# Kernel tuning notes

Hardware: AMD Instinct MI355X
Metric: run time of the kernel (lower is better)

## Reference

```python
import jax, jax.numpy as jnp
import numpy as np

N_EMBD = 1024
N_HEAD = 16
HEAD_DIM = N_EMBD // N_HEAD
B, T = 8, 1024


def setup_inputs() -> dict:
    key = jax.random.key(0)
    k1, k2, k3, k4 = jax.random.split(key, 4)
    x = jax.random.normal(k1, (B, T, N_EMBD), dtype=jnp.float32)
    # nn.Linear weight shapes: qkv (3C, C) no bias; proj (C, C) with bias
    w_qkv = jax.random.normal(k2, (3 * N_EMBD, N_EMBD), dtype=jnp.float32) * 0.02
    w_proj = jax.random.normal(k3, (N_EMBD, N_EMBD), dtype=jnp.float32) * 0.02
    b_proj = jax.random.normal(k4, (N_EMBD,), dtype=jnp.float32) * 0.02
    return {"x": x, "w_qkv": w_qkv, "w_proj": w_proj, "b_proj": b_proj}


def reference(x, w_qkv, w_proj, b_proj):
    Bq, Tq, C = x.shape
    qkv = jnp.einsum('btc,dc->btd', x, w_qkv)  # (B,T,3C)
    q, k, v = jnp.split(qkv, 3, axis=-1)
    def heads(t):
        return t.reshape(Bq, Tq, N_HEAD, HEAD_DIM).transpose(0, 2, 1, 3)  # (B,H,T,D)
    q, k, v = heads(q), heads(k), heads(v)
    scale = 1.0 / np.sqrt(HEAD_DIM).astype(np.float32)
    att = jnp.einsum('bhqd,bhkd->bhqk', q, k) * scale  # (B,H,T,T)
    causal = jnp.tril(jnp.ones((Tq, Tq), dtype=bool))
    att = jnp.where(causal, att, -jnp.inf)
    att = jax.nn.softmax(att, axis=-1)
    # dropout: eval mode -> identity
    y = jnp.einsum('bhqk,bhkd->bhqd', att, v)
    y = y.transpose(0, 2, 1, 3).reshape(Bq, Tq, C)
    return jnp.einsum('btc,dc->btd', y, w_proj) + b_proj
```

## Files before the change

### kernel.cpp

```cpp
#include <hip/hip_runtime.h>
#include <stdint.h>


#define Bn 8
#define Tn 1024
#define Cn 1024
#define Hn 16
#define Dn 64
#define Mn (Bn * Tn)
#define NQKV (3 * Cn)
#define QKS 2048

typedef unsigned short u16;
typedef float f32x4 __attribute__((ext_vector_type(4)));
typedef __bf16 bf16x8 __attribute__((ext_vector_type(8)));
typedef unsigned short ushx8 __attribute__((ext_vector_type(8)));
typedef unsigned short ushx4 __attribute__((ext_vector_type(4)));

__device__ __forceinline__ u16 f2bf(float f) {
  unsigned int u = __float_as_uint(f);
  u += 0x7fffu + ((u >> 16) & 1u);
  return (u16)(u >> 16);
}
__device__ __forceinline__ u16 f2bf_rna(float f) {
  return (u16)((__float_as_uint(f) + 0x8000u) >> 16);
}

__device__ __forceinline__ f32x4 mfma_bf16(ushx8 a, ushx8 b, f32x4 c) {
  return __builtin_amdgcn_mfma_f32_16x16x32_bf16(
      __builtin_bit_cast(bf16x8, a), __builtin_bit_cast(bf16x8, b), c, 0, 0, 0);
}

__device__ __forceinline__ void async16(const u16* g, u16* l) {
  __builtin_amdgcn_global_load_lds(
      (__attribute__((address_space(1))) void*)(void*)g,
      (__attribute__((address_space(3))) void*)l, 16, 0, 0);
}

template <int CTRL>
__device__ __forceinline__ float dppmov(float v) {
  return __builtin_bit_cast(float, __builtin_amdgcn_update_dpp(
      0, __builtin_bit_cast(int, v), CTRL, 0xf, 0xf, true));
}
__device__ __forceinline__ float red16max(float v) {
  v = fmaxf(v, dppmov<0xB1>(v));
  v = fmaxf(v, dppmov<0x4E>(v));
  v = fmaxf(v, dppmov<0x141>(v));
  v = fmaxf(v, dppmov<0x140>(v));
  return v;
}
__device__ __forceinline__ float red16sum(float v) {
  v += dppmov<0xB1>(v);
  v += dppmov<0x4E>(v);
  v += dppmov<0x141>(v);
  v += dppmov<0x140>(v);
  return v;
}

__global__ void cast3_kernel(const float* __restrict__ a, u16* __restrict__ oa, int na4,
                             const float* __restrict__ b, u16* __restrict__ ob, int nb4,
                             const float* __restrict__ c, u16* __restrict__ oc, int nc4) {
  int i = blockIdx.x * blockDim.x + threadIdx.x;
  const float* in;
  u16* out;
  if (i < na4) { in = a; out = oa; }
  else if (i < na4 + nb4) { in = b; out = ob; i -= na4; }
  else if (i < na4 + nb4 + nc4) { in = c; out = oc; i -= na4 + nb4; }
  else return;
  float4 v = ((const float4*)in)[i];
  ushx4 o = { f2bf(v.x), f2bf(v.y), f2bf(v.z), f2bf(v.w) };
  ((ushx4*)out)[i] = o;
}

#define SLOG2E 0.18033688011112042f

template <int MODE>
__device__ __forceinline__ void gemm_body(
    const u16* __restrict__ A, const u16* __restrict__ Bw,
    void* __restrict__ Cout, u16* __restrict__ vt,
    const float* __restrict__ bias) {
  __shared__ alignas(16) u16 lds[36864];

  const int tid = threadIdx.x;
  const int lane = tid & 63;
  const int wv = tid >> 6;
  const int quad = lane >> 4;
  const int l16 = lane & 15;
  const int wr = wv >> 1;
  const int wc = wv & 1;

  const int xcd = blockIdx.x & 7;
  const int loc = blockIdx.x >> 3;
  const int m0 = (xcd * 4 + (loc & 3)) * 256;
  const int n0 = (loc >> 2) * 128;

  const u16* gA = A + (size_t)m0 * Cn;
  const u16* gB = Bw + (size_t)n0 * Cn;

  const int r0s = tid >> 2;
  const int q0s = (tid & 3) ^ ((r0s >> 1) & 3);
  const int c1s = 512 + tid;
  const int r1s = c1s >> 2;
  const int q1s = (c1s & 3) ^ ((r1s >> 1) & 3);
  const int so0 = r0s * Cn + q0s * 8;
  const int so1 = r1s * Cn + q1s * 8;

  auto stageA = [&](int slot, int h) {
    u16* dst = lds + slot * 8192 + tid * 8;
    const u16* src = gA + (h >> 1) * 64 + (h & 1) * 32;
    async16(src + so0, dst);
    async16(src + so1, dst + 4096);
  };
  auto stageB = [&](int slot, int h) {
    u16* dst = lds + 24576 + slot * 4096 + tid * 8;
    const u16* src = gB + (h >> 1) * 64 + (h & 1) * 32;
    async16(src + so0, dst);
  };

  const int sread = (quad ^ ((l16 >> 1) & 3)) * 8;
  const int aoff = (wr * 64 + l16) * 32 + sread;
  const int boff = 24576 + (wc * 64 + l16) * 32 + sread;

  f32x4 acc[4][4];
#pragma unroll
  for (int i = 0; i < 4; ++i)
#pragma unroll
    for (int j = 0; j < 4; ++j) acc[i][j] = (f32x4){0.f, 0.f, 0.f, 0.f};
  ushx8 af[4], bfr[4];

  stageA(0, 0); stageB(0, 0);
  stageA(1, 1); stageB(1, 1);
  asm volatile("s_waitcnt vmcnt(3)" ::: "memory");
  __builtin_amdgcn_s_barrier();
  asm volatile("" ::: "memory");

#define PH(slot, sslot, hd)                                                    \
  {                                                                            \
    const u16* ab_ = lds + (slot) * 8192 + aoff;                               \
    af[0] = *(const ushx8*)(ab_);                                              \
    af[1] = *(const ushx8*)(ab_ + 512);                                        \
    af[2] = *(const ushx8*)(ab_ + 1024);                                       \
    af[3] = *(const ushx8*)(ab_ + 1536);                                       \
    const u16* bb_ = lds + (slot) * 4096 + boff;                               \
    bfr[0] = *(const ushx8*)(bb_);                                             \
    bfr[1] = *(const ushx8*)(bb_ + 512);                                       \
    bfr[2] = *(const ushx8*)(bb_ + 1024);                                      \
    bfr[3] = *(const ushx8*)(bb_ + 1536);                                      \
    stageA((sslot), (hd));                                                     \
    stageB((sslot), (hd));                                                     \
    asm volatile("" ::: "memory");                                             \
    __builtin_amdgcn_s_barrier();                                              \
    asm volatile("s_waitcnt lgkmcnt(0)" ::: "memory");                         \
    __builtin_amdgcn_s_setprio(1);                                             \
    _Pragma("unroll") for (int mi_ = 0; mi_ < 4; ++mi_) {                      \
      _Pragma("unroll") for (int ni_ = 0; ni_ < 4; ++ni_) {                    \
        acc[mi_][ni_] = mfma_bf16(af[mi_], bfr[ni_], acc[mi_][ni_]);           \
      }                                                                        \
    }                                                                          \
    __builtin_amdgcn_s_setprio(0);                                             \
    asm volatile("s_waitcnt vmcnt(3)" ::: "memory");                           \
    asm volatile("" ::: "memory");                                             \
    __builtin_amdgcn_s_barrier();                                              \
    asm volatile("" ::: "memory");                                             \
  }

#pragma unroll 1
  for (int it = 0; it < 5; ++it) {
    const int p = it * 6;
    PH(0, 2, p + 2)
    PH(1, 0, p + 3)
    PH(2, 1, p + 4)
    PH(0, 2, p + 5)
    PH(1, 0, p + 6)
    PH(2, 1, p + 7)
  }
  PH(0, 2, 31)
  PH(1, 0, 31)
#undef PH
  asm volatile("s_waitcnt vmcnt(0)" ::: "memory");

  if constexpr (MODE) {
    if (n0 < 2 * Cn) {
      const float sc = (n0 < Cn) ? SLOG2E : 1.f;
#pragma unroll
      for (int mi = 0; mi < 4; ++mi) {
#pragma unroll
        for (int ni = 0; ni < 4; ++ni) {
          const int col = n0 + wc * 64 + ni * 16 + l16;
          const int row = m0 + wr * 64 + mi * 16 + quad * 4;
#pragma unroll
          for (int i = 0; i < 4; ++i)
            ((u16*)Cout)[(size_t)(row + i) * QKS + col] = f2bf(acc[mi][ni][i] * sc);
        }
      }
    } else {
#pragma unroll
      for (int mi = 0; mi < 4; ++mi) {
#pragma unroll
        for (int ni = 0; ni < 4; ++ni) {
          const int colV = n0 - 2 * Cn + wc * 64 + ni * 16 + l16;
          const int hh = colV >> 6, dd = colV & 63;
          const int row0 = m0 + wr * 64 + mi * 16 + quad * 4;
          const int bb = row0 >> 10, tt = row0 & 1023;
          unsigned int lo = (unsigned int)f2bf(acc[mi][ni][0]) |
                            ((unsigned int)f2bf(acc[mi][ni][1]) << 16);
          unsigned int hi = (unsigned int)f2bf(acc[mi][ni][2]) |
                            ((unsigned int)f2bf(acc[mi][ni][3]) << 16);
          uint2 pk = {lo, hi};
          *(uint2*)&vt[((size_t)(bb * Hn + hh) * Dn + dd) * Tn + tt] = pk;
        }
      }
    }
  } else {
#pragma unroll
    for (int mi = 0; mi < 4; ++mi) {
#pragma unroll
      for (int ni = 0; ni < 4; ++ni) {
        const int col = n0 + wc * 64 + ni * 16 + l16;
        const float bv = bias[col];
        const int row = m0 + wr * 64 + mi * 16 + quad * 4;
#pragma unroll
        for (int i = 0; i < 4; ++i)
          ((float*)Cout)[(size_t)(row + i) * Cn + col] = acc[mi][ni][i] + bv;
      }
    }
  }
}

__global__ __launch_bounds__(512, 4) void gemm_qkv_k(
    const u16* __restrict__ A, const u16* __restrict__ Bw,
    u16* __restrict__ qk, u16* __restrict__ vt) {
  gemm_body<1>(A, Bw, (void*)qk, vt, nullptr);
}
__global__ __launch_bounds__(512, 4) void gemm_proj_k(
    const u16* __restrict__ A, const u16* __restrict__ Bw,
    float* __restrict__ out, const float* __restrict__ bias) {
  gemm_body<0>(A, Bw, (void*)out, nullptr, bias);
}

__global__ __launch_bounds__(512, 4) void attn_kernel(
    const u16* __restrict__ qk, const u16* __restrict__ vt,
    u16* __restrict__ out) {
  const int j = blockIdx.x, h = blockIdx.y, b = blockIdx.z;
  const int tid = threadIdx.x;
  const int lane = tid & 63;
  const int wv = tid >> 6;
  const int quad = lane >> 4;
  const int l16 = lane & 15;

  __shared__ alignas(16) u16 Ks[2][64 * 64];
  __shared__ alignas(16) u16 Vts[2][64 * 64];
  __shared__ alignas(16) u16 Ps[8][16 * 72];

  const u16* qb = qk + (size_t)b * Tn * QKS + h * Dn;
  const u16* kb = qk + (size_t)b * Tn * QKS + Cn + h * Dn;
  const u16* vtb = vt + (size_t)(b * Hn + h) * Dn * Tn;

  const int srow = tid >> 3;
  const int scc = tid & 7;
  const int sgc = scc ^ (srow & 7);
  u16* pswv = Ps[wv];

#pragma unroll 1
  for (int ph = 0; ph < 2; ++ph) {
    const int qt = ph ? (7 - j) : j;
    const int q0w = qt * 128 + wv * 16;
    const int ntiles = 2 * qt + 2;
    const int tdiag = q0w >> 6;

    ushx8 qf[2];
    {
      const u16* qp = qb + (size_t)(q0w + l16) * QKS + quad * 8;
      qf[0] = *(const ushx8*)qp;
      qf[1] = *(const ushx8*)(qp + 32);
    }

    f32x4 o[4];
#pragma unroll
    for (int nt = 0; nt < 4; ++nt) o[nt] = (f32x4){0.f, 0.f, 0.f, 0.f};
    float mrow[4], lrow[4];
#pragma unroll
    for (int i = 0; i < 4; ++i) { mrow[i] = -__builtin_inff(); lrow[i] = 0.f; }

    __syncthreads();

    async16(kb + (size_t)srow * QKS + sgc * 8, Ks[0] + tid * 8);
    async16(vtb + (size_t)srow * Tn + sgc * 8, Vts[0] + tid * 8);

#pragma unroll 1
    for (int t = 0; t < ntiles; ++t) {
      const int kv0 = t * 64;
      const int bi = t & 1;
      __syncthreads();

      if (t + 1 < ntiles) {
        const int nkv0 = kv0 + 64;
        async16(kb + (size_t)(nkv0 + srow) * QKS + sgc * 8, Ks[bi ^ 1] + tid * 8);
        async16(vtb + (size_t)srow * Tn + nkv0 + sgc * 8, Vts[bi ^ 1] + tid * 8);
      }

      if (t > tdiag) continue;

      const u16* ks = Ks[bi];
      const u16* vs = Vts[bi];
      f32x4 s[4];
#pragma unroll
      for (int nt = 0; nt < 4; ++nt) s[nt] = (f32x4){0.f, 0.f, 0.f, 0.f};
#pragma unroll
      for (int nt = 0; nt < 4; ++nt) {
        const int rb = nt * 16 + l16;
        ushx8 b0 = *(const ushx8*)(ks + rb * 64 + (quad ^ (rb & 7)) * 8);
        ushx8 b1 = *(const ushx8*)(ks + rb * 64 + ((quad + 4) ^ (rb & 7)) * 8);
        s[nt] = mfma_bf16(qf[0], b0, s[nt]);
        s[nt] = mfma_bf16(qf[1], b1, s[nt]);
      }

      if (t == tdiag) {
#pragma unroll
        for (int i = 0; i < 4; ++i) {
          const int qr = q0w + quad * 4 + i;
          float vv[4];
          float rmax = -__builtin_inff();
#pragma unroll
          for (int nt = 0; nt < 4; ++nt) {
            float v = s[nt][i];
            if ((kv0 + nt * 16 + l16) > qr) v = -__builtin_inff();
            vv[nt] = v;
            rmax = fmaxf(rmax, v);
          }
          rmax = red16max(rmax);
          const float mnew = fmaxf(mrow[i], rmax);
          const float al = __builtin_amdgcn_exp2f(mrow[i] - mnew);
          mrow[i] = mnew;
          float rsum = 0.f;
#pragma unroll
          for (int nt = 0; nt < 4; ++nt) {
            float p = __builtin_amdgcn_exp2f(vv[nt] - mnew);
            rsum += p;
            pswv[(quad * 4 + i) * 72 + nt * 16 + l16] = f2bf_rna(p);
          }
          lrow[i] = lrow[i] * al + rsum;
#pragma unroll
          for (int nt = 0; nt < 4; ++nt) o[nt][i] *= al;
        }
      } else {
#pragma unroll
        for (int i = 0; i < 4; ++i) {
          float rmax = fmaxf(fmaxf(s[0][i], s[1][i]), fmaxf(s[2][i], s[3][i]));
          rmax = red16max(rmax);
          const float mnew = fmaxf(mrow[i], rmax);
          const float al = __builtin_amdgcn_exp2f(mrow[i] - mnew);
          mrow[i] = mnew;
          float rsum = 0.f;
#pragma unroll
          for (int nt = 0; nt < 4; ++nt) {
            float p = __builtin_amdgcn_exp2f(s[nt][i] - mnew);
            rsum += p;
            pswv[(quad * 4 + i) * 72 + nt * 16 + l16] = f2bf_rna(p);
          }
          lrow[i] = lrow[i] * al + rsum;
#pragma unroll
          for (int nt = 0; nt < 4; ++nt) o[nt][i] *= al;
        }
      }

      ushx8 pf0, pf1;
      {
        const u16* pp = pswv + l16 * 72 + quad * 8;
        pf0 = *(const ushx8*)pp;
        pf1 = *(const ushx8*)(pp + 32);
      }

#pragma unroll
      for (int nt = 0; nt < 4; ++nt) {
        const int rb = nt * 16 + l16;
        ushx8 v0 = *(const ushx8*)(vs + rb * 64 + (quad ^ (rb & 7)) * 8);
        ushx8 v1 = *(const ushx8*)(vs + rb * 64 + ((quad + 4) ^ (rb & 7)) * 8);
        o[nt] = mfma_bf16(pf0, v0, o[nt]);
        o[nt] = mfma_bf16(pf1, v1, o[nt]);
      }
    }

#pragma unroll
    for (int i = 0; i < 4; ++i) {
      const float inv = 1.f / red16sum(lrow[i]);
      const int trow = q0w + quad * 4 + i;
      u16* op = out + ((size_t)(b * Tn + trow)) * Cn + h * Dn + l16;
#pragma unroll
      for (int nt = 0; nt < 4; ++nt) op[nt * 16] = f2bf(o[nt][i] * inv);
    }
  }
}

extern "C" void kernel_launch(void* const* d_in, const int* in_sizes, int n_in,
                              void* d_out, int out_size, void* d_ws, size_t ws_size,
                              hipStream_t stream) {
  const float* x = (const float*)d_in[0];
  const float* w_qkv = (const float*)d_in[1];
  const float* w_proj = (const float*)d_in[2];
  const float* b_proj = (const float*)d_in[3];
  float* out = (float*)d_out;
  char* ws = (char*)d_ws;

  u16* xb     = (u16*)(ws);
  u16* wqkvb  = (u16*)(ws + 16777216);
  u16* wprojb = (u16*)(ws + 23068672);
  u16* qkb    = (u16*)(ws + 25165824);
  u16* vtb    = (u16*)(ws + 58720256);
  u16* yb     = (u16*)(ws + 75497472);

  cast3_kernel<<<12288, 256, 0, stream>>>(x, xb, 2097152,
                                          w_qkv, wqkvb, 786432,
                                          w_proj, wprojb, 262144);

  gemm_qkv_k<<<768, 512, 0, stream>>>(xb, wqkvb, qkb, vtb);

  attn_kernel<<<dim3(4, Hn, Bn), 512, 0, stream>>>(qkb, vtb, yb);

  gemm_proj_k<<<256, 512, 0, stream>>>(yb, wprojb, out, b_proj);
}
```

Before: 224.3 us.

## Use 4-wave GEMM blocks with larger per-wave tiles and smaller proj tiles

```diff
diff --git a/kernel.cpp b/kernel.cpp
--- a/kernel.cpp
+++ b/kernel.cpp
@@ -74,12 +74,22 @@
 
 #define SLOG2E 0.18033688011112042f
 
-template <int MODE>
-__device__ __forceinline__ void gemm_body(
+template <int BM, int MODE>
+__device__ __forceinline__ void gemm_body4(
     const u16* __restrict__ A, const u16* __restrict__ Bw,
     void* __restrict__ Cout, u16* __restrict__ vt,
     const float* __restrict__ bias) {
-  __shared__ alignas(16) u16 lds[36864];
+  constexpr int ASLOT = BM * 32;
+  constexpr int BSLOT = 128 * 32;
+  constexpr int BBASE = 3 * ASLOT;
+  constexpr int ASW = BM / 64;
+  constexpr int BSW = 2;
+  constexpr int LOADS = ASW + BSW;
+  constexpr int MREP = BM / 32;
+  constexpr int MT = Mn / BM;
+  constexpr int MPX = MT / 8;
+
+  __shared__ alignas(16) u16 lds[3 * (ASLOT + BSLOT)];
 
   const int tid = threadIdx.x;
   const int lane = tid & 63;
@@ -91,74 +101,73 @@
 
   const int xcd = blockIdx.x & 7;
   const int loc = blockIdx.x >> 3;
-  const int m0 = (xcd * 4 + (loc & 3)) * 256;
-  const int n0 = (loc >> 2) * 128;
+  const int m0 = (xcd * MPX + (loc & (MPX - 1))) * BM;
+  const int n0 = (loc / MPX) * 128;
 
   const u16* gA = A + (size_t)m0 * Cn;
   const u16* gB = Bw + (size_t)n0 * Cn;
 
-  const int r0s = tid >> 2;
-  const int q0s = (tid & 3) ^ ((r0s >> 1) & 3);
-  const int c1s = 512 + tid;
-  const int r1s = c1s >> 2;
-  const int q1s = (c1s & 3) ^ ((r1s >> 1) & 3);
-  const int so0 = r0s * Cn + q0s * 8;
-  const int so1 = r1s * Cn + q1s * 8;
-
-  auto stageA = [&](int slot, int h) {
-    u16* dst = lds + slot * 8192 + tid * 8;
-    const u16* src = gA + (h >> 1) * 64 + (h & 1) * 32;
-    async16(src + so0, dst);
-    async16(src + so1, dst + 4096);
+  int soff[4];
+#pragma unroll
+  for (int s = 0; s < 4; ++s) {
+    int c = s * 256 + tid;
+    int row = c >> 2;
+    int q = (c & 3) ^ ((row >> 1) & 3);
+    soff[s] = row * Cn + q * 8;
+  }
+
+  auto stage = [&](int slot, int h) {
+    const u16* sA = gA + (h >> 1) * 64 + (h & 1) * 32;
+    u16* dA = lds + slot * ASLOT + tid * 8;
+#pragma unroll
+    for (int s = 0; s < ASW; ++s) async16(sA + soff[s], dA + s * 2048);
+    const u16* sB = gB + (h >> 1) * 64 + (h & 1) * 32;
+    u16* dB = lds + BBASE + slot * BSLOT + tid * 8;
+#pragma unroll
+    for (int s = 0; s < BSW; ++s) async16(sB + soff[s], dB + s * 2048);
   };
-  auto stageB = [&](int slot, int h) {
-    u16* dst = lds + 24576 + slot * 4096 + tid * 8;
-    const u16* src = gB + (h >> 1) * 64 + (h & 1) * 32;
-    async16(src + so0, dst);
-  };
 
   const int sread = (quad ^ ((l16 >> 1) & 3)) * 8;
-  const int aoff = (wr * 64 + l16) * 32 + sread;
-  const int boff = 24576 + (wc * 64 + l16) * 32 + sread;
-
-  f32x4 acc[4][4];
-#pragma unroll
-  for (int i = 0; i < 4; ++i)
+  const int aoff = (wr * (BM / 2) + l16) * 32 + sread;
+  const int boff = BBASE + (wc * 64 + l16) * 32 + sread;
+
+  f32x4 acc[MREP][4];
+#pragma unroll
+  for (int i = 0; i < MREP; ++i)
 #pragma unroll
     for (int j = 0; j < 4; ++j) acc[i][j] = (f32x4){0.f, 0.f, 0.f, 0.f};
-  ushx8 af[4], bfr[4];
-
-  stageA(0, 0); stageB(0, 0);
-  stageA(1, 1); stageB(1, 1);
-  asm volatile("s_waitcnt vmcnt(3)" ::: "memory");
+  ushx8 af[MREP], bfr[4];
+
+  stage(0, 0);
+  stage(1, 1);
+  if constexpr (LOADS == 6) asm volatile("s_waitcnt vmcnt(6)" ::: "memory");
+  else asm volatile("s_waitcnt vmcnt(4)" ::: "memory");
   __builtin_amdgcn_s_barrier();
   asm volatile("" ::: "memory");
 
 #define PH(slot, sslot, hd)                                                    \
   {                                                                            \
-    const u16* ab_ = lds + (slot) * 8192 + aoff;                               \
-    af[0] = *(const ushx8*)(ab_);                                              \
-    af[1] = *(const ushx8*)(ab_ + 512);                                        \
-    af[2] = *(const ushx8*)(ab_ + 1024);                                       \
-    af[3] = *(const ushx8*)(ab_ + 1536);                                       \
-    const u16* bb_ = lds + (slot) * 4096 + boff;                               \
-    bfr[0] = *(const ushx8*)(bb_);                                             \
-    bfr[1] = *(const ushx8*)(bb_ + 512);                                       \
-    bfr[2] = *(const ushx8*)(bb_ + 1024);                                      \
-    bfr[3] = *(const ushx8*)(bb_ + 1536);                                      \
-    stageA((sslot), (hd));                                                     \
-    stageB((sslot), (hd));                                                     \
+    const u16* ab_ = lds + (slot) * ASLOT + aoff;                              \
+    _Pragma("unroll") for (int mi_ = 0; mi_ < MREP; ++mi_)                     \
+      af[mi_] = *(const ushx8*)(ab_ + mi_ * 512);                              \
+    const u16* bb_ = lds + (slot) * BSLOT + boff;                              \
+    _Pragma("unroll") for (int ni_ = 0; ni_ < 4; ++ni_)                        \
+      bfr[ni_] = *(const ushx8*)(bb_ + ni_ * 512);                             \
+    stage((sslot), (hd));                                                      \
     asm volatile("" ::: "memory");                                             \
     __builtin_amdgcn_s_barrier();                                              \
     asm volatile("s_waitcnt lgkmcnt(0)" ::: "memory");                         \
     __builtin_amdgcn_s_setprio(1);                                             \
-    _Pragma("unroll") for (int mi_ = 0; mi_ < 4; ++mi_) {                      \
+    _Pragma("unroll") for (int mi_ = 0; mi_ < MREP; ++mi_) {                   \
       _Pragma("unroll") for (int ni_ = 0; ni_ < 4; ++ni_) {                    \
         acc[mi_][ni_] = mfma_bf16(af[mi_], bfr[ni_], acc[mi_][ni_]);           \
       }                                                                        \
     }                                                                          \
     __builtin_amdgcn_s_setprio(0);                                             \
-    asm volatile("s_waitcnt vmcnt(3)" ::: "memory");                           \
+    if constexpr (LOADS == 6)                                                  \
+      asm volatile("s_waitcnt vmcnt(6)" ::: "memory");                         \
+    else                                                                       \
+      asm volatile("s_waitcnt vmcnt(4)" ::: "memory");                         \
     asm volatile("" ::: "memory");                                             \
     __builtin_amdgcn_s_barrier();                                              \
     asm volatile("" ::: "memory");                                             \
@@ -183,11 +192,11 @@
     if (n0 < 2 * Cn) {
       const float sc = (n0 < Cn) ? SLOG2E : 1.f;
 #pragma unroll
-      for (int mi = 0; mi < 4; ++mi) {
+      for (int mi = 0; mi < MREP; ++mi) {
 #pragma unroll
         for (int ni = 0; ni < 4; ++ni) {
           const int col = n0 + wc * 64 + ni * 16 + l16;
-          const int row = m0 + wr * 64 + mi * 16 + quad * 4;
+          const int row = m0 + wr * (BM / 2) + mi * 16 + quad * 4;
 #pragma unroll
           for (int i = 0; i < 4; ++i)
             ((u16*)Cout)[(size_t)(row + i) * QKS + col] = f2bf(acc[mi][ni][i] * sc);
@@ -195,12 +204,12 @@
       }
     } else {
 #pragma unroll
-      for (int mi = 0; mi < 4; ++mi) {
+      for (int mi = 0; mi < MREP; ++mi) {
 #pragma unroll
         for (int ni = 0; ni < 4; ++ni) {
           const int colV = n0 - 2 * Cn + wc * 64 + ni * 16 + l16;
           const int hh = colV >> 6, dd = colV & 63;
-          const int row0 = m0 + wr * 64 + mi * 16 + quad * 4;
+          const int row0 = m0 + wr * (BM / 2) + mi * 16 + quad * 4;
           const int bb = row0 >> 10, tt = row0 & 1023;
           unsigned int lo = (unsigned int)f2bf(acc[mi][ni][0]) |
                             ((unsigned int)f2bf(acc[mi][ni][1]) << 16);
@@ -213,12 +222,12 @@
     }
   } else {
 #pragma unroll
-    for (int mi = 0; mi < 4; ++mi) {
+    for (int mi = 0; mi < MREP; ++mi) {
 #pragma unroll
       for (int ni = 0; ni < 4; ++ni) {
         const int col = n0 + wc * 64 + ni * 16 + l16;
         const float bv = bias[col];
-        const int row = m0 + wr * 64 + mi * 16 + quad * 4;
+        const int row = m0 + wr * (BM / 2) + mi * 16 + quad * 4;
 #pragma unroll
         for (int i = 0; i < 4; ++i)
           ((float*)Cout)[(size_t)(row + i) * Cn + col] = acc[mi][ni][i] + bv;
@@ -227,15 +236,15 @@
   }
 }
 
-__global__ __launch_bounds__(512, 4) void gemm_qkv_k(
+__global__ __launch_bounds__(256, 2) void gemm_qkv_k(
     const u16* __restrict__ A, const u16* __restrict__ Bw,
     u16* __restrict__ qk, u16* __restrict__ vt) {
-  gemm_body<1>(A, Bw, (void*)qk, vt, nullptr);
-}
-__global__ __launch_bounds__(512, 4) void gemm_proj_k(
+  gemm_body4<256, 1>(A, Bw, (void*)qk, vt, nullptr);
+}
+__global__ __launch_bounds__(256, 2) void gemm_proj_k(
     const u16* __restrict__ A, const u16* __restrict__ Bw,
     float* __restrict__ out, const float* __restrict__ bias) {
-  gemm_body<0>(A, Bw, (void*)out, nullptr, bias);
+  gemm_body4<128, 0>(A, Bw, (void*)out, nullptr, bias);
 }
 
 __global__ __launch_bounds__(512, 4) void attn_kernel(
@@ -413,9 +422,9 @@
                                           w_qkv, wqkvb, 786432,
                                           w_proj, wprojb, 262144);
 
-  gemm_qkv_k<<<768, 512, 0, stream>>>(xb, wqkvb, qkb, vtb);
+  gemm_qkv_k<<<768, 256, 0, stream>>>(xb, wqkvb, qkb, vtb);
 
   attn_kernel<<<dim3(4, Hn, Bn), 512, 0, stream>>>(qkb, vtb, yb);
 
-  gemm_proj_k<<<256, 512, 0, stream>>>(yb, wprojb, out, b_proj);
-}
+  gemm_proj_k<<<512, 256, 0, stream>>>(yb, wprojb, out, b_proj);
+}
```

After: 220.1 us. No clear change (-1.9%).
